# Kernel tuning notes

Hardware: AMD Instinct MI355X
Metric: run time of the kernel (lower is better)

## Reference

```python
import jax, jax.numpy as jnp
import numpy as np

NUM_HEADS = 8


def setup_inputs() -> dict:
    key = jax.random.key(0)
    ks = jax.random.split(key, 16)
    B, Ct, Co, H, W = 1, 256, 128, 64, 64
    s = lambda k, *shape: jax.random.normal(k, shape, dtype=jnp.float32) * 0.02
    return {
        "thermal_features": jax.random.normal(ks[0], (B, Ct, H, W), dtype=jnp.float32),
        "optical_features": jax.random.normal(ks[1], (B, Co, H, W), dtype=jnp.float32),
        "emissivity_map": jax.random.uniform(ks[2], (B, 1, H, W), dtype=jnp.float32),
        "Wq": s(ks[3], Ct, Ct), "bq": jnp.zeros((Ct,), jnp.float32),
        "Wk": s(ks[4], Ct, Co), "bk": jnp.zeros((Ct,), jnp.float32),
        "Wv": s(ks[5], Ct, Co), "bv": jnp.zeros((Ct,), jnp.float32),
        "conv1_w": s(ks[6], 32, 1, 3, 3), "conv1_b": jnp.zeros((32,), jnp.float32),
        "conv2_w": s(ks[7], NUM_HEADS, 32, 1, 1), "conv2_b": jnp.zeros((NUM_HEADS,), jnp.float32),
        "Wp": s(ks[8], Ct, Ct), "bp": jnp.zeros((Ct,), jnp.float32),
    }


def reference(thermal_features, optical_features, emissivity_map,
              Wq, bq, Wk, bk, Wv, bv, conv1_w, conv1_b, conv2_w, conv2_b, Wp, bp):
    B, Ct, H, W = thermal_features.shape
    Co = optical_features.shape[1]
    N = H * W
    h = NUM_HEADS
    d = Ct // h
    scale = d ** (-0.5)

    # flatten spatial -> tokens: [B, N, C]
    t_flat = thermal_features.reshape(B, Ct, N).transpose(0, 2, 1)
    o_flat = optical_features.reshape(B, Co, N).transpose(0, 2, 1)

    # projections, split heads: [B, h, N, d]
    q = (t_flat @ Wq.T + bq).reshape(B, N, h, d).transpose(0, 2, 1, 3)
    k = (o_flat @ Wk.T + bk).reshape(B, N, h, d).transpose(0, 2, 1, 3)
    v = (o_flat @ Wv.T + bv).reshape(B, N, h, d).transpose(0, 2, 1, 3)

    # full attention scores: [B, h, N, N]
    attn = jnp.einsum('bhqd,bhkd->bhqk', q, k) * scale

    # emissivity gate: Conv(1->32, 3x3, pad 1) -> ReLU -> Conv(32->h, 1x1) -> Sigmoid
    g = jax.lax.conv_general_dilated(emissivity_map, conv1_w, (1, 1), 'SAME',
                                     dimension_numbers=('NCHW', 'OIHW', 'NCHW'))
    g = jax.nn.relu(g + conv1_b[None, :, None, None])
    g = jax.lax.conv_general_dilated(g, conv2_w, (1, 1), 'SAME',
                                     dimension_numbers=('NCHW', 'OIHW', 'NCHW'))
    g = jax.nn.sigmoid(g + conv2_b[None, :, None, None])  # [B, h, H, W]
    g = g.reshape(B, h, N)[..., None]  # [B, h, N, 1] gates query rows

    attn = jax.nn.softmax(attn * g, axis=-1)  # dropout is identity in eval

    out = jnp.einsum('bhqk,bhkd->bhqd', attn, v)  # [B, h, N, d]
    out = out.transpose(0, 2, 1, 3).reshape(B, N, Ct)
    out = out @ Wp.T + bp
    return out.transpose(0, 2, 1).reshape(B, Ct, H, W)
```

## Files before the change

### kernel.cpp

```cpp
#include <hip/hip_runtime.h>
#include <hip/hip_bf16.h>

#define N_TOK 4096
#define CT 256

typedef __attribute__((ext_vector_type(8))) short bf16x8;
typedef __attribute__((ext_vector_type(16))) float f32x16;

__device__ __forceinline__ unsigned pkbf(float a, float b) {
  float2 t; t.x = a; t.y = b;
  __hip_bfloat162 h = __float22bfloat162_rn(t);
  return *reinterpret_cast<unsigned*>(&h);
}

#if __has_builtin(__builtin_amdgcn_exp2f)
__device__ __forceinline__ float fexp2(float x) { return __builtin_amdgcn_exp2f(x); }
#else
__device__ __forceinline__ float fexp2(float x) { return exp2f(x); }
#endif

__global__ __launch_bounds__(256) void prep_kernel(
    const float* __restrict__ thermal, const float* __restrict__ optical,
    const float* __restrict__ Wq, const float* __restrict__ Wk,
    const float* __restrict__ Wv, const float* __restrict__ Wp,
    const float* __restrict__ em, const float* __restrict__ w1,
    const float* __restrict__ b1, const float* __restrict__ w2,
    const float* __restrict__ b2,
    unsigned short* __restrict__ Xbt, unsigned short* __restrict__ Xbo,
    unsigned short* __restrict__ Wall, float* __restrict__ g)
{
  __shared__ unsigned short tile[64][264];
  const int bx = blockIdx.x, tid = threadIdx.x;
  if (bx < 128) {
    const bool th = (bx < 64);
    const float* X = th ? thermal : optical;
    unsigned short* Xb = th ? Xbt : Xbo;
    const int CIN = th ? 256 : 128;
    const int n0 = (th ? bx : bx - 64) * 64;
    const int nl = tid & 63;
    const int cw = (tid >> 6) * 4;
    for (int c0 = 0; c0 < CIN; c0 += 16) {
      int c = c0 + cw;
      float x0 = X[(size_t)(c + 0) * N_TOK + n0 + nl];
      float x1 = X[(size_t)(c + 1) * N_TOK + n0 + nl];
      float x2 = X[(size_t)(c + 2) * N_TOK + n0 + nl];
      float x3 = X[(size_t)(c + 3) * N_TOK + n0 + nl];
      uint2 w; w.x = pkbf(x0, x1); w.y = pkbf(x2, x3);
      *(uint2*)&tile[nl][c] = w;
    }
    __syncthreads();
    const int n = tid >> 2, q = tid & 3;
    const int cb = q * (CIN / 4);
    for (int j = 0; j < CIN / 4; j += 4)
      *(uint2*)(Xb + (size_t)(n0 + n) * CIN + cb + j) = *(const uint2*)&tile[n][cb + j];
  } else if (bx < 224) {
    int i = (bx - 128) * 2048 + tid * 8;
    const float* src; int off;
    if (i < 65536)       { src = Wq; off = 0; }
    else if (i < 98304)  { src = Wk; off = 65536; }
    else if (i < 131072) { src = Wv; off = 98304; }
    else                 { src = Wp; off = 131072; }
    float4 f0 = *(const float4*)(src + (i - off));
    float4 f1 = *(const float4*)(src + (i - off) + 4);
    uint4 o;
    o.x = pkbf(f0.x, f0.y); o.y = pkbf(f0.z, f0.w);
    o.z = pkbf(f1.x, f1.y); o.w = pkbf(f1.z, f1.w);
    *(uint4*)(Wall + i) = o;
  } else {
    int n = (bx - 224) * 256 + tid;
    int y = n >> 6, x = n & 63;
    float e[9];
#pragma unroll
    for (int dy = 0; dy < 3; dy++)
#pragma unroll
      for (int dx = 0; dx < 3; dx++) {
        int yy = y + dy - 1, xx = x + dx - 1;
        e[dy * 3 + dx] = (yy >= 0 && yy < 64 && xx >= 0 && xx < 64)
                             ? em[yy * 64 + xx] : 0.f;
      }
    float c1[32];
#pragma unroll
    for (int oc = 0; oc < 32; oc++) {
      float a = b1[oc];
#pragma unroll
      for (int t = 0; t < 9; t++) a = fmaf(e[t], w1[oc * 9 + t], a);
      c1[oc] = fmaxf(a, 0.f);
    }
#pragma unroll
    for (int hh = 0; hh < 8; hh++) {
      float a = b2[hh];
#pragma unroll
      for (int oc = 0; oc < 32; oc++) a = fmaf(c1[oc], w2[hh * 32 + oc], a);
      g[hh * N_TOK + n] = 1.f / (1.f + __expf(-a));
    }
  }
}

template <int CIN>
__device__ __forceinline__ void gemm_tile(
    const unsigned short* __restrict__ xp, const unsigned short* __restrict__ wp,
    f32x16& accE, f32x16& accO)
{
#pragma unroll
  for (int c = 0; c < CIN; c += 32) {
    bf16x8 a0 = *(const bf16x8*)(xp + c);
    bf16x8 b0 = *(const bf16x8*)(wp + c);
    bf16x8 a1 = *(const bf16x8*)(xp + c + 16);
    bf16x8 b1 = *(const bf16x8*)(wp + c + 16);
    accE = __builtin_amdgcn_mfma_f32_32x32x16_bf16(a0, b0, accE, 0, 0, 0);
    accO = __builtin_amdgcn_mfma_f32_32x32x16_bf16(a1, b1, accO, 0, 0, 0);
  }
}

__global__ __launch_bounds__(256) void qkv_kernel(
    const unsigned short* __restrict__ Xbt, const unsigned short* __restrict__ Xbo,
    const unsigned short* __restrict__ Wall,
    const float* __restrict__ bq, const float* __restrict__ bk,
    const float* __restrict__ bv, const float* __restrict__ g,
    unsigned short* __restrict__ Qh, unsigned short* __restrict__ Kh,
    unsigned short* __restrict__ Vf)
{
  __shared__ float ldsT[4][32][33];
  const int tid = threadIdx.x;
  const int wave = tid >> 6, lane = tid & 63;
  const int l31 = lane & 31, hi = lane >> 5;
  const int y = blockIdx.y;
  const int head = y & 7;
  const int n0 = blockIdx.x * 128 + wave * 32;

  f32x16 accE, accO;
#pragma unroll
  for (int i = 0; i < 16; i++) { accE[i] = 0.f; accO[i] = 0.f; }
  float bo;
  if (y < 8) {
    gemm_tile<256>(Xbt + (size_t)(n0 + l31) * 256 + hi * 8,
                   Wall + (size_t)(head * 32 + l31) * 256 + hi * 8, accE, accO);
    bo = bq[head * 32 + l31];
  } else if (y < 16) {
    gemm_tile<128>(Xbo + (size_t)(n0 + l31) * 128 + hi * 8,
                   Wall + 65536 + (size_t)(head * 32 + l31) * 128 + hi * 8, accE, accO);
    bo = bk[head * 32 + l31];
  } else {
    gemm_tile<128>(Xbo + (size_t)(n0 + l31) * 128 + hi * 8,
                   Wall + 98304 + (size_t)(head * 32 + l31) * 128 + hi * 8, accE, accO);
    bo = bv[head * 32 + l31];
  }
  float val[16];
#pragma unroll
  for (int r = 0; r < 16; r++) val[r] = accE[r] + accO[r] + bo;

  if (y < 8) {
    const float QSC = 0.17677669529663689f * 1.4426950408889634f;
#pragma unroll
    for (int r = 0; r < 16; r++) {
      int t = n0 + (r & 3) + 8 * (r >> 2) + 4 * hi;
      val[r] *= QSC * g[head * N_TOK + t];
    }
  }
#pragma unroll
  for (int r = 0; r < 16; r++)
    ldsT[wave][(r & 3) + 8 * (r >> 2) + 4 * hi][l31] = val[r];

  if (y < 16) {
    unsigned pk[8];
#pragma unroll
    for (int i = 0; i < 8; i++)
      pk[i] = pkbf(ldsT[wave][l31][16 * hi + 2 * i],
                   ldsT[wave][l31][16 * hi + 2 * i + 1]);
    unsigned short* dst = (y < 8 ? Qh : Kh) +
        ((size_t)head * N_TOK + n0 + l31) * 32 + 16 * hi;
    *(uint4*)dst = make_uint4(pk[0], pk[1], pk[2], pk[3]);
    *(uint4*)(dst + 8) = make_uint4(pk[4], pk[5], pk[6], pk[7]);
  } else {
    unsigned pk[8];
#pragma unroll
    for (int i = 0; i < 8; i++)
      pk[i] = pkbf(ldsT[wave][16 * hi + 2 * i][l31],
                   ldsT[wave][16 * hi + 2 * i + 1][l31]);
    unsigned short* dst = Vf +
        (((size_t)head * 256 + (n0 >> 4) + hi) * 32 + l31) * 16;
    *(uint4*)dst = make_uint4(pk[0], pk[1], pk[2], pk[3]);
    *(uint4*)(dst + 8) = make_uint4(pk[4], pk[5], pk[6], pk[7]);
  }
}

__global__ __launch_bounds__(256, 4) void attn_kernel(
    const unsigned short* __restrict__ Qh, const unsigned short* __restrict__ Kh,
    const unsigned short* __restrict__ Vf, unsigned short* __restrict__ Ab)
{
  __shared__ float combA[4][32][33];
  __shared__ float combL[4][32];
  const int tid = threadIdx.x;
  const int wave = tid >> 6, lane = tid & 63;
  const int l31 = lane & 31, hi = lane >> 5;
  const int hh = blockIdx.x & 7;
  const int qb = blockIdx.x >> 3;
  const int qrow0 = qb * 32;
  const int kbase0 = wave * 1024;

  const unsigned short* qrow = Qh + ((size_t)hh * N_TOK + qrow0 + l31) * 32;
  const bf16x8 qf0 = *(const bf16x8*)(qrow + hi * 8);
  const bf16x8 qf1 = *(const bf16x8*)(qrow + 16 + hi * 8);

  const unsigned short* kb_base = Kh + (size_t)hh * (N_TOK * 32);
  const unsigned short* vf_base = Vf + (size_t)hh * (256 * 32 * 16);

  f32x16 acc, zero16;
#pragma unroll
  for (int i = 0; i < 16; i++) { acc[i] = 0.f; zero16[i] = 0.f; }
  float lsum = 0.f;

#define LK(kb, s) (*(const bf16x8*)(kb_base + (size_t)((kb) + l31) * 32 + (s) * 16 + hi * 8))
#define LV(kt2)   (*(const bf16x8*)(vf_base + (size_t)((kt2) * 32 + l31) * 16 + hi * 8))

  bf16x8 kf0 = LK(kbase0, 0), kf1 = LK(kbase0, 1);
  bf16x8 vb0 = LV(kbase0 >> 4), vb1 = LV((kbase0 >> 4) + 1);

#pragma unroll 2
  for (int kt = 0; kt < 1024; kt += 32) {
    const int nxt = (kt + 32 < 1024) ? (kbase0 + kt + 32) : kbase0;
    bf16x8 nk0 = LK(nxt, 0), nk1 = LK(nxt, 1);
    bf16x8 nv0 = LV(nxt >> 4), nv1 = LV((nxt >> 4) + 1);

    f32x16 s = __builtin_amdgcn_mfma_f32_32x32x16_bf16(kf0, qf0, zero16, 0, 0, 0);
    s = __builtin_amdgcn_mfma_f32_32x32x16_bf16(kf1, qf1, s, 0, 0, 0);

    float p[16];
#pragma unroll
    for (int r = 0; r < 16; r++) p[r] = fexp2(s[r]);

    lsum += (((p[0] + p[1]) + (p[2] + p[3])) + ((p[4] + p[5]) + (p[6] + p[7]))) +
            (((p[8] + p[9]) + (p[10] + p[11])) + ((p[12] + p[13]) + (p[14] + p[15])));

    unsigned a0 = pkbf(p[0], p[1]),   a1 = pkbf(p[2], p[3]);
    unsigned b0 = pkbf(p[4], p[5]),   b1 = pkbf(p[6], p[7]);
    unsigned c0 = pkbf(p[8], p[9]),   c1 = pkbf(p[10], p[11]);
    unsigned d0 = pkbf(p[12], p[13]), d1 = pkbf(p[14], p[15]);
    asm("v_permlane32_swap_b32 %0, %1" : "+v"(a0), "+v"(b0));
    asm("v_permlane32_swap_b32 %0, %1" : "+v"(a1), "+v"(b1));
    asm("v_permlane32_swap_b32 %0, %1" : "+v"(c0), "+v"(d0));
    asm("v_permlane32_swap_b32 %0, %1" : "+v"(c1), "+v"(d1));
    union { unsigned w[4]; bf16x8 v; } u0, u1;
    u0.w[0] = a0; u0.w[1] = a1; u0.w[2] = b0; u0.w[3] = b1;
    u1.w[0] = c0; u1.w[1] = c1; u1.w[2] = d0; u1.w[3] = d1;

    acc = __builtin_amdgcn_mfma_f32_32x32x16_bf16(u0.v, vb0, acc, 0, 0, 0);
    acc = __builtin_amdgcn_mfma_f32_32x32x16_bf16(u1.v, vb1, acc, 0, 0, 0);

    kf0 = nk0; kf1 = nk1; vb0 = nv0; vb1 = nv1;
  }
#undef LK
#undef LV

  float lt = lsum + __shfl_xor(lsum, 32);
  if (hi == 0) combL[wave][l31] = lt;

#pragma unroll
  for (int r = 0; r < 16; r++)
    combA[wave][(r & 3) + 8 * (r >> 2) + 4 * hi][l31] = acc[r];
  __syncthreads();

  const int t = tid >> 3;
  const int c4 = (tid & 7) * 4;
  float l = combL[0][t] + combL[1][t] + combL[2][t] + combL[3][t];
  float inv = 1.f / l;
  float o[4];
#pragma unroll
  for (int j = 0; j < 4; j++)
    o[j] = combA[0][t][c4 + j] + combA[1][t][c4 + j] +
           combA[2][t][c4 + j] + combA[3][t][c4 + j];
  uint2 pk;
  pk.x = pkbf(o[0] * inv, o[1] * inv);
  pk.y = pkbf(o[2] * inv, o[3] * inv);
  *(uint2*)(Ab + (size_t)(qrow0 + t) * CT + hh * 32 + c4) = pk;
}

__global__ __launch_bounds__(256) void pout_kernel(
    const unsigned short* __restrict__ Ab, const unsigned short* __restrict__ Wall,
    const float* __restrict__ bp, float* __restrict__ out)
{
  const int tid = threadIdx.x;
  const int wave = tid >> 6, lane = tid & 63;
  const int l31 = lane & 31, hi = lane >> 5;
  const int n0 = blockIdx.x * 128 + wave * 32;
  const int o0 = blockIdx.y * 32;

  f32x16 accE, accO;
#pragma unroll
  for (int i = 0; i < 16; i++) { accE[i] = 0.f; accO[i] = 0.f; }
  gemm_tile<256>(Ab + (size_t)(n0 + l31) * 256 + hi * 8,
                 Wall + 131072 + (size_t)(o0 + l31) * 256 + hi * 8, accE, accO);
  const float bo = bp[o0 + l31];
#pragma unroll
  for (int rr = 0; rr < 4; rr++) {
    float4 w = make_float4(accE[4 * rr + 0] + accO[4 * rr + 0] + bo,
                           accE[4 * rr + 1] + accO[4 * rr + 1] + bo,
                           accE[4 * rr + 2] + accO[4 * rr + 2] + bo,
                           accE[4 * rr + 3] + accO[4 * rr + 3] + bo);
    *(float4*)(out + (size_t)(o0 + l31) * N_TOK + n0 + 8 * rr + 4 * hi) = w;
  }
}

extern "C" void kernel_launch(void* const* d_in, const int* in_sizes, int n_in,
                              void* d_out, int out_size, void* d_ws, size_t ws_size,
                              hipStream_t stream)
{
  const float* thermal = (const float*)d_in[0];
  const float* optical = (const float*)d_in[1];
  const float* em      = (const float*)d_in[2];
  const float* Wq = (const float*)d_in[3];
  const float* bq = (const float*)d_in[4];
  const float* Wk = (const float*)d_in[5];
  const float* bk = (const float*)d_in[6];
  const float* Wv = (const float*)d_in[7];
  const float* bv = (const float*)d_in[8];
  const float* w1 = (const float*)d_in[9];
  const float* b1 = (const float*)d_in[10];
  const float* w2 = (const float*)d_in[11];
  const float* b2 = (const float*)d_in[12];
  const float* Wp = (const float*)d_in[13];
  const float* bp = (const float*)d_in[14];

  char* ws = (char*)d_ws;
  const size_t MB = 1u << 20;
  unsigned short* Xbt = (unsigned short*)(ws);
  unsigned short* Xbo = (unsigned short*)(ws + 2 * MB);
  unsigned short* Wall = (unsigned short*)(ws + 3 * MB);
  float* gbuf = (float*)(ws + 3 * MB + 512 * 1024);
  unsigned short* Qh = (unsigned short*)(ws + 4 * MB);
  unsigned short* Kh = (unsigned short*)(ws + 6 * MB);
  unsigned short* Vf = (unsigned short*)(ws + 8 * MB);
  unsigned short* Ab = (unsigned short*)(ws + 10 * MB);

  prep_kernel<<<240, 256, 0, stream>>>(thermal, optical, Wq, Wk, Wv, Wp,
                                       em, w1, b1, w2, b2, Xbt, Xbo, Wall, gbuf);
  qkv_kernel<<<dim3(32, 24), 256, 0, stream>>>(Xbt, Xbo, Wall, bq, bk, bv, gbuf,
                                               Qh, Kh, Vf);
  attn_kernel<<<1024, 256, 0, stream>>>(Qh, Kh, Vf, Ab);
  pout_kernel<<<dim3(32, 8), 256, 0, stream>>>(Ab, Wall, bp, (float*)d_out);
}
```

Before: 60.29 us.

## Split output projection K across waves and raise MFMA priority in attention

```diff
diff --git a/kernel.cpp b/kernel.cpp
--- a/kernel.cpp
+++ b/kernel.cpp
@@ -222,8 +222,10 @@
     bf16x8 nk0 = LK(nxt, 0), nk1 = LK(nxt, 1);
     bf16x8 nv0 = LV(nxt >> 4), nv1 = LV((nxt >> 4) + 1);
 
+    __builtin_amdgcn_s_setprio(1);
     f32x16 s = __builtin_amdgcn_mfma_f32_32x32x16_bf16(kf0, qf0, zero16, 0, 0, 0);
     s = __builtin_amdgcn_mfma_f32_32x32x16_bf16(kf1, qf1, s, 0, 0, 0);
+    __builtin_amdgcn_s_setprio(0);
 
     float p[16];
 #pragma unroll
@@ -244,8 +246,10 @@
     u0.w[0] = a0; u0.w[1] = a1; u0.w[2] = b0; u0.w[3] = b1;
     u1.w[0] = c0; u1.w[1] = c1; u1.w[2] = d0; u1.w[3] = d1;
 
+    __builtin_amdgcn_s_setprio(1);
     acc = __builtin_amdgcn_mfma_f32_32x32x16_bf16(u0.v, vb0, acc, 0, 0, 0);
     acc = __builtin_amdgcn_mfma_f32_32x32x16_bf16(u1.v, vb1, acc, 0, 0, 0);
+    __builtin_amdgcn_s_setprio(0);
 
     kf0 = nk0; kf1 = nk1; vb0 = nv0; vb1 = nv1;
   }
@@ -275,30 +279,47 @@
   *(uint2*)(Ab + (size_t)(qrow0 + t) * CT + hh * 32 + c4) = pk;
 }
 
-__global__ __launch_bounds__(256) void pout_kernel(
+__global__ __launch_bounds__(256, 4) void pout_kernel(
     const unsigned short* __restrict__ Ab, const unsigned short* __restrict__ Wall,
     const float* __restrict__ bp, float* __restrict__ out)
 {
+  __shared__ float comb[4][32][33];
   const int tid = threadIdx.x;
   const int wave = tid >> 6, lane = tid & 63;
   const int l31 = lane & 31, hi = lane >> 5;
-  const int n0 = blockIdx.x * 128 + wave * 32;
+  const int n0 = blockIdx.x * 32;
   const int o0 = blockIdx.y * 32;
+  const int cbase = wave * 64;
+
+  const unsigned short* xp = Ab + (size_t)(n0 + l31) * 256 + cbase + hi * 8;
+  const unsigned short* wp = Wall + 131072 + (size_t)(o0 + l31) * 256 + cbase + hi * 8;
 
   f32x16 accE, accO;
 #pragma unroll
   for (int i = 0; i < 16; i++) { accE[i] = 0.f; accO[i] = 0.f; }
-  gemm_tile<256>(Ab + (size_t)(n0 + l31) * 256 + hi * 8,
-                 Wall + 131072 + (size_t)(o0 + l31) * 256 + hi * 8, accE, accO);
-  const float bo = bp[o0 + l31];
-#pragma unroll
-  for (int rr = 0; rr < 4; rr++) {
-    float4 w = make_float4(accE[4 * rr + 0] + accO[4 * rr + 0] + bo,
-                           accE[4 * rr + 1] + accO[4 * rr + 1] + bo,
-                           accE[4 * rr + 2] + accO[4 * rr + 2] + bo,
-                           accE[4 * rr + 3] + accO[4 * rr + 3] + bo);
-    *(float4*)(out + (size_t)(o0 + l31) * N_TOK + n0 + 8 * rr + 4 * hi) = w;
-  }
+#pragma unroll
+  for (int c = 0; c < 64; c += 32) {
+    bf16x8 a0 = *(const bf16x8*)(xp + c);
+    bf16x8 b0 = *(const bf16x8*)(wp + c);
+    bf16x8 a1 = *(const bf16x8*)(xp + c + 16);
+    bf16x8 b1 = *(const bf16x8*)(wp + c + 16);
+    accE = __builtin_amdgcn_mfma_f32_32x32x16_bf16(a0, b0, accE, 0, 0, 0);
+    accO = __builtin_amdgcn_mfma_f32_32x32x16_bf16(a1, b1, accO, 0, 0, 0);
+  }
+#pragma unroll
+  for (int r = 0; r < 16; r++)
+    comb[wave][(r & 3) + 8 * (r >> 2) + 4 * hi][l31] = accE[r] + accO[r];
+  __syncthreads();
+
+  const int oc = tid >> 3;
+  const int t4 = (tid & 7) * 4;
+  const float bo = bp[o0 + oc];
+  float4 w;
+  w.x = comb[0][t4 + 0][oc] + comb[1][t4 + 0][oc] + comb[2][t4 + 0][oc] + comb[3][t4 + 0][oc] + bo;
+  w.y = comb[0][t4 + 1][oc] + comb[1][t4 + 1][oc] + comb[2][t4 + 1][oc] + comb[3][t4 + 1][oc] + bo;
+  w.z = comb[0][t4 + 2][oc] + comb[1][t4 + 2][oc] + comb[2][t4 + 2][oc] + comb[3][t4 + 2][oc] + bo;
+  w.w = comb[0][t4 + 3][oc] + comb[1][t4 + 3][oc] + comb[2][t4 + 3][oc] + comb[3][t4 + 3][oc] + bo;
+  *(float4*)(out + (size_t)(o0 + oc) * N_TOK + n0 + t4) = w;
 }
 
 extern "C" void kernel_launch(void* const* d_in, const int* in_sizes, int n_in,
@@ -337,5 +358,5 @@
   qkv_kernel<<<dim3(32, 24), 256, 0, stream>>>(Xbt, Xbo, Wall, bq, bk, bv, gbuf,
                                                Qh, Kh, Vf);
   attn_kernel<<<1024, 256, 0, stream>>>(Qh, Kh, Vf, Ab);
-  pout_kernel<<<dim3(32, 8), 256, 0, stream>>>(Ab, Wall, bp, (float*)d_out);
-}
+  pout_kernel<<<dim3(128, 8), 256, 0, stream>>>(Ab, Wall, bp, (float*)d_out);
+}
```

Measured after the change: 59.80 us. Within noise of the previous version (-0.8%).
